# Performance work log

Measured on AMD Instinct MI355X. Metric: run time of the kernel, lower is better.

The kernel has to match this reference:

```python
import jax, jax.numpy as jnp
import numpy as np

B, T, S = 1, 8, 1024
HID, H = 1152, 16
D = HID // H  # 72
EPS = 1e-6


def rmsnorm(t, gamma):
    # t: [b,t,s,h,d], gamma: [h,d] per-head learnable scale (QKNorm)
    var = jnp.mean(jnp.square(t), axis=-1, keepdims=True)
    return t * jax.lax.rsqrt(var + EPS) * gamma


def setup_inputs() -> dict:
    key = jax.random.key(0)
    ks = jax.random.split(key, 8)
    sc = lambda fan_in: 1.0 / np.sqrt(fan_in)
    x = jax.random.normal(ks[0], (B, T, S, HID), dtype=jnp.float32)
    Wq = jax.random.normal(ks[1], (HID, HID), dtype=jnp.float32) * sc(HID)
    bq = jnp.zeros((HID,), dtype=jnp.float32)
    Wkv = jax.random.normal(ks[2], (HID, 2 * HID), dtype=jnp.float32) * sc(HID)
    bkv = jnp.zeros((2 * HID,), dtype=jnp.float32)
    q_gamma = jnp.ones((H, D), dtype=jnp.float32)
    k_gamma = jnp.ones((H, D), dtype=jnp.float32)
    Wo = jax.random.normal(ks[3], (HID, HID), dtype=jnp.float32) * sc(HID)
    return {"x": x, "Wq": Wq, "bq": bq, "Wkv": Wkv, "bkv": bkv,
            "q_gamma": q_gamma, "k_gamma": k_gamma, "Wo": Wo}


def reference(x, Wq, bq, Wkv, bkv, q_gamma, k_gamma, Wo):
    b, t, s, _ = x.shape
    q = (x @ Wq + bq).reshape(b, t, s, H, D)
    kv = x @ Wkv + bkv
    k, v = jnp.split(kv, 2, axis=-1)
    k = k.reshape(b, t, s, H, D)
    v = v.reshape(b, t, s, H, D)
    q = rmsnorm(q, q_gamma)
    k = rmsnorm(k, k_gamma)
    # NOTE: original applies no 1/sqrt(d) scaling (QKNorm replaces it)
    attn_weight = jnp.einsum('btqhd,btkhd->bthqk', q, k)
    attn = jax.nn.softmax(attn_weight, axis=-1)
    out = jnp.einsum('bthqk,btkhd->btqhd', attn, v).reshape(b, t, s, HID)
    return out @ Wo
```

## Files before the change

### kernel.cpp

```cpp
#include <hip/hip_runtime.h>


typedef __attribute__((ext_vector_type(4))) short s16x4;
typedef __attribute__((ext_vector_type(8))) short s16x8;
typedef __attribute__((ext_vector_type(4))) float f32x4;
typedef __attribute__((ext_vector_type(16))) float f32x16;
typedef __attribute__((ext_vector_type(4))) int i32x4;

__device__ __forceinline__ unsigned short f2b(float x) {
  unsigned u = __float_as_uint(x);
  u += 0x7FFFu + ((u >> 16) & 1u);
  return (unsigned short)(u >> 16);
}
__device__ __forceinline__ float b2f(unsigned short u) {
  return __uint_as_float(((unsigned)u) << 16);
}
__device__ __forceinline__ void gld16(const void* g, void* l) {
  __builtin_amdgcn_global_load_lds(
      (const __attribute__((address_space(1))) void*)g,
      (__attribute__((address_space(3))) void*)l, 16, 0, 0);
}

__global__ __launch_bounds__(256) void cvt_bf16_kernel(const float* __restrict__ in,
                                                       unsigned short* __restrict__ out,
                                                       int n16) {
  int i = blockIdx.x * 256 + threadIdx.x;
  if (i >= n16) return;
  const float4* p = (const float4*)(in + (size_t)i * 16);
  float4 a = p[0], b = p[1], c = p[2], d = p[3];
  s16x8 r0, r1;
  r0[0] = (short)f2b(a.x); r0[1] = (short)f2b(a.y); r0[2] = (short)f2b(a.z); r0[3] = (short)f2b(a.w);
  r0[4] = (short)f2b(c.x); r0[5] = (short)f2b(c.y); r0[6] = (short)f2b(c.z); r0[7] = (short)f2b(c.w);
  r1[0] = (short)f2b(b.x); r1[1] = (short)f2b(b.y); r1[2] = (short)f2b(b.z); r1[3] = (short)f2b(b.w);
  r1[4] = (short)f2b(d.x); r1[5] = (short)f2b(d.y); r1[6] = (short)f2b(d.z); r1[7] = (short)f2b(d.w);
  *(s16x8*)(out + (size_t)i * 16) = r0;
  *(s16x8*)(out + (size_t)i * 16 + 8) = r1;
}

__global__ __launch_bounds__(256) void transpose_cvt_kernel(const float* __restrict__ W,
                                                            unsigned short* __restrict__ WT,
                                                            int K, int N) {
  __shared__ float tile[32][33];
  int n0 = blockIdx.x * 32, k0 = blockIdx.y * 32;
  int tx = threadIdx.x, ty = threadIdx.y;
#pragma unroll
  for (int i = 0; i < 4; i++)
    tile[ty + i * 8][tx] = W[(size_t)(k0 + ty + i * 8) * N + n0 + tx];
  __syncthreads();
  int stx = (tx & 19) | ((tx & 4) << 1) | ((tx & 8) >> 1);
#pragma unroll
  for (int i = 0; i < 4; i++)
    WT[(size_t)(n0 + ty + i * 8) * K + k0 + stx] = f2b(tile[tx][ty + i * 8]);
}

__global__ __launch_bounds__(256) void gemm_qkv_kernel(const unsigned short* __restrict__ A,
                                                       const unsigned short* __restrict__ BT,
                                                       const float* __restrict__ biasq,
                                                       const float* __restrict__ biaskv,
                                                       unsigned short* __restrict__ qn,
                                                       unsigned short* __restrict__ kn,
                                                       unsigned short* __restrict__ vt) {
  constexpr int K = 1152;
  constexpr int NT = K / 32;
  __shared__ __align__(16) unsigned short LDSU[3 * 8192 + 3 * 4096];
  unsigned short* As = LDSU;
  unsigned short* Bs = LDSU + 3 * 8192;
  int tid = threadIdx.x;
  int lane = tid & 63, wave = tid >> 6;
  int wr = (wave >> 1) * 128, wc = (wave & 1) * 64;
  int l31 = lane & 31, lh = lane >> 5;
  int bid = blockIdx.x;
  int xcd = bid & 7;
  int w = bid >> 3;
  int st = w / 12, inner = w - st * 12;
  int ibx = inner % 3, iby = inner / 3;
  int bx = st * 3 + ibx;
  int by = xcd * 4 + iby;
  int brow = by * 256, bcol = bx * 128;
  const unsigned short* AsrcP[4];
  const unsigned short* BsrcP[2];
  int dstA[4], dstB[2];
#pragma unroll
  for (int i = 0; i < 4; i++) {
    int c = tid + 256 * i;
    int row = c >> 2, j = c & 3;
    AsrcP[i] = A + (size_t)(brow + row) * K + (j ^ ((row >> 1) & 3)) * 8;
    dstA[i] = (wave * 64 + 256 * i) * 8;
  }
#pragma unroll
  for (int i = 0; i < 2; i++) {
    int c = tid + 256 * i;
    int row = c >> 2, j = c & 3;
    BsrcP[i] = BT + (size_t)(bcol + row) * K + (j ^ ((row >> 1) & 3)) * 8;
    dstB[i] = (wave * 64 + 256 * i) * 8;
  }
#define STAGE(KT, BUF)                                           \
  {                                                              \
    int kb = (KT) * 32;                                          \
    gld16(AsrcP[0] + kb, &As[(BUF) * 8192 + dstA[0]]);           \
    gld16(AsrcP[1] + kb, &As[(BUF) * 8192 + dstA[1]]);           \
    gld16(AsrcP[2] + kb, &As[(BUF) * 8192 + dstA[2]]);           \
    gld16(AsrcP[3] + kb, &As[(BUF) * 8192 + dstA[3]]);           \
    gld16(BsrcP[0] + kb, &Bs[(BUF) * 4096 + dstB[0]]);           \
    gld16(BsrcP[1] + kb, &Bs[(BUF) * 4096 + dstB[1]]);           \
  }
  int fr = (l31 >> 1) & 3;
  int slotk[2] = {(lh ^ fr) * 8, ((2 + lh) ^ fr) * 8};
  STAGE(0, 0);
  STAGE(1, 1);
  f32x16 acc[4][2] = {};
  int cur = 0;
  for (int kt = 0; kt < NT; kt++) {
    if (kt < NT - 1)
      asm volatile("s_waitcnt vmcnt(6)\n\ts_barrier" ::: "memory");
    else
      asm volatile("s_waitcnt vmcnt(0)\n\ts_barrier" ::: "memory");
    if (kt + 2 < NT) {
      int nb = (cur == 0) ? 2 : cur - 1;
      STAGE(kt + 2, nb);
    }
    int ab = cur * 8192, bb = cur * 4096;
#pragma unroll
    for (int kk = 0; kk < 2; kk++) {
      int so = slotk[kk];
      s16x8 af[4], bf[2];
#pragma unroll
      for (int m = 0; m < 4; m++)
        af[m] = *(const s16x8*)&As[ab + (wr + m * 32 + l31) * 32 + so];
#pragma unroll
      for (int n = 0; n < 2; n++)
        bf[n] = *(const s16x8*)&Bs[bb + (wc + n * 32 + l31) * 32 + so];
      __builtin_amdgcn_s_setprio(1);
#pragma unroll
      for (int m = 0; m < 4; m++)
#pragma unroll
        for (int n = 0; n < 2; n++)
          acc[m][n] = __builtin_amdgcn_mfma_f32_32x32x16_bf16(af[m], bf[n], acc[m][n], 0, 0, 0);
      __builtin_amdgcn_s_setprio(0);
    }
    cur = (cur == 2) ? 0 : cur + 1;
  }
#undef STAGE
  if (bcol >= 2304) {
    __syncthreads();
    int c0 = bcol - 2304;
#pragma unroll
    for (int m = 0; m < 4; m++) {
#pragma unroll
      for (int n = 0; n < 2; n++) {
        int col = wc + n * 32 + l31;
        float bias = biaskv[1152 + c0 + col];
#pragma unroll
        for (int reg = 0; reg < 16; reg++) {
          int row = wr + m * 32 + (reg & 3) + 8 * (reg >> 2) + 4 * lh;
          LDSU[col * 264 + row] = f2b(acc[m][n][reg] + bias);
        }
      }
    }
    __syncthreads();
    int t = brow >> 10, sbase = brow & 1023;
#pragma unroll
    for (int i = 0; i < 16; i++) {
      int id = tid + 256 * i;
      int col = id >> 5, rowc = id & 31;
      int c = c0 + col;
      int h = c / 72, d = c - h * 72;
      s16x8 v8 = *(const s16x8*)&LDSU[col * 264 + rowc * 8];
      *(s16x8*)(vt + ((size_t)((t * 16 + h) * 80 + d)) * 1024 + sbase + rowc * 8) = v8;
    }
  } else {
#pragma unroll
    for (int m = 0; m < 4; m++) {
#pragma unroll
      for (int n = 0; n < 2; n++) {
        int gcol = bcol + wc + n * 32 + l31;
        float bias = (gcol < 1152) ? biasq[gcol] : biaskv[gcol - 1152];
        int c = (gcol < 1152) ? gcol : gcol - 1152;
        int h = c / 72, d = c - h * 72;
        unsigned short* dst = (gcol < 1152) ? qn : kn;
#pragma unroll
        for (int reg = 0; reg < 16; reg++) {
          int grow = brow + wr + m * 32 + (reg & 3) + 8 * (reg >> 2) + 4 * lh;
          float v = acc[m][n][reg] + bias;
          int t = grow >> 10, s = grow & 1023;
          dst[((size_t)((t * 16 + h) * 1024 + s)) * 96 + d] = f2b(v);
        }
      }
    }
  }
}

__global__ __launch_bounds__(256) void gemm_out_kernel(const unsigned short* __restrict__ A,
                                                       const unsigned short* __restrict__ BT,
                                                       int N, int gx,
                                                       float* __restrict__ outF) {
  constexpr int K = 1152;
  constexpr int NT = K / 32;
  __shared__ __align__(16) unsigned short As[3 * 4096];
  __shared__ __align__(16) unsigned short Bs[3 * 4096];
  int tid = threadIdx.x;
  int lane = tid & 63, wave = tid >> 6;
  int wr = (wave >> 1) * 64, wc = (wave & 1) * 64;
  int l31 = lane & 31, lh = lane >> 5;
  int bid = blockIdx.x;
  int xcd = bid & 7;
  int w = bid >> 3;
  int st = w / 24, inner = w - st * 24;
  int ibx = inner % 3, iby = inner / 3;
  int bx = st * 3 + ibx;
  int by = xcd * 8 + iby;
  int brow = by * 128, bcol = bx * 128;
  const unsigned short* AsrcP[2];
  const unsigned short* BsrcP[2];
  int dst0[2];
#pragma unroll
  for (int i = 0; i < 2; i++) {
    int c = tid + 256 * i;
    int row = c >> 2, j = c & 3;
    int ch = j ^ ((row >> 1) & 3);
    AsrcP[i] = A + (size_t)(brow + row) * K + ch * 8;
    BsrcP[i] = BT + (size_t)(bcol + row) * K + ch * 8;
    dst0[i] = (wave * 64 + 256 * i) * 8;
  }
#define STAGE(KT, BUF)                                          \
  {                                                             \
    int kb = (KT) * 32;                                         \
    gld16(AsrcP[0] + kb, &As[(BUF) * 4096 + dst0[0]]);          \
    gld16(BsrcP[0] + kb, &Bs[(BUF) * 4096 + dst0[0]]);          \
    gld16(AsrcP[1] + kb, &As[(BUF) * 4096 + dst0[1]]);          \
    gld16(BsrcP[1] + kb, &Bs[(BUF) * 4096 + dst0[1]]);          \
  }
  int fr = (l31 >> 1) & 3;
  int slotk[2] = {(lh ^ fr) * 8, ((2 + lh) ^ fr) * 8};
  STAGE(0, 0);
  STAGE(1, 1);
  f32x16 acc[2][2] = {};
  int cur = 0;
  for (int kt = 0; kt < NT; kt++) {
    if (kt < NT - 1)
      asm volatile("s_waitcnt vmcnt(4)\n\ts_barrier" ::: "memory");
    else
      asm volatile("s_waitcnt vmcnt(0)\n\ts_barrier" ::: "memory");
    if (kt + 2 < NT) {
      int nb = (cur == 0) ? 2 : cur - 1;
      STAGE(kt + 2, nb);
    }
    int ab = cur * 4096;
#pragma unroll
    for (int kk = 0; kk < 2; kk++) {
      int so = slotk[kk];
      s16x8 af[2], bf[2];
#pragma unroll
      for (int m = 0; m < 2; m++)
        af[m] = *(const s16x8*)&As[ab + (wr + m * 32 + l31) * 32 + so];
#pragma unroll
      for (int n = 0; n < 2; n++)
        bf[n] = *(const s16x8*)&Bs[ab + (wc + n * 32 + l31) * 32 + so];
      __builtin_amdgcn_s_setprio(1);
#pragma unroll
      for (int m = 0; m < 2; m++)
#pragma unroll
        for (int n = 0; n < 2; n++)
          acc[m][n] = __builtin_amdgcn_mfma_f32_32x32x16_bf16(af[m], bf[n], acc[m][n], 0, 0, 0);
      __builtin_amdgcn_s_setprio(0);
    }
    cur = (cur == 2) ? 0 : cur + 1;
  }
#undef STAGE
#pragma unroll
  for (int m = 0; m < 2; m++) {
#pragma unroll
    for (int n = 0; n < 2; n++) {
#pragma unroll
      for (int reg = 0; reg < 16; reg++) {
        int grow = brow + wr + m * 32 + (reg & 3) + 8 * (reg >> 2) + 4 * lh;
        int gcol = bcol + wc + n * 32 + l31;
        outF[(size_t)grow * N + gcol] = acc[m][n][reg];
      }
    }
  }
}

__global__ __launch_bounds__(256) void rmsnorm2_kernel(unsigned short* __restrict__ qn,
                                                       unsigned short* __restrict__ kn,
                                                       const float* __restrict__ qg,
                                                       const float* __restrict__ kg) {
  int r = blockIdx.x * 4 + (threadIdx.x >> 6);
  int isK = r >= 131072;
  int g = isK ? r - 131072 : r;
  unsigned short* buf = isK ? kn : qn;
  const float* gamma = isK ? kg : qg;
  int h = (g >> 10) & 15;
  size_t base = (size_t)g * 96;
  int l = threadIdx.x & 63;
  float e0 = b2f(buf[base + l]);
  float e1 = 0.f;
  if (l < 8) e1 = b2f(buf[base + 64 + l]);
  float ss = e0 * e0 + e1 * e1;
#pragma unroll
  for (int m = 1; m < 64; m <<= 1) ss += __shfl_xor(ss, m);
  float sc = rsqrtf(ss * (1.0f / 72.0f) + 1e-6f);
  buf[base + l] = f2b(e0 * sc * gamma[h * 72 + l]);
  if (l < 32) {
    float v = 0.f;
    if (l < 8) v = e1 * sc * gamma[h * 72 + 64 + l];
    buf[base + 64 + l] = f2b(v);
  }
}

__global__ __launch_bounds__(256) void attn_kernel(const unsigned short* __restrict__ Qn,
                                                   const unsigned short* __restrict__ Kn,
                                                   const unsigned short* __restrict__ VtG,
                                                   unsigned short* __restrict__ att) {
  __shared__ unsigned short Kl[2][64][100];
  __shared__ unsigned short Vt[2][80][76];
  int tid = threadIdx.x;
  int lane = tid & 63, wave = tid >> 6;
  int l15 = lane & 15, lq = lane >> 4, kf = lq * 4;
  int bid = blockIdx.x;
  int orig = (bid & 7) * 128 + (bid >> 3);
  int qb = orig & 7, th = orig >> 3;
  int t = th >> 4, h = th & 15;
  const unsigned short* Q = Qn + (size_t)th * 1024 * 96;
  const unsigned short* Kp = Kn + (size_t)th * 1024 * 96;
  const unsigned short* Vg = VtG + (size_t)th * 80 * 1024;
  int qrow0 = qb * 128 + wave * 32;
  int krow[3], kco[3], vd[3], vco[3];
#pragma unroll
  for (int i = 0; i < 3; i++) {
    int c = tid + i * 256;
    krow[i] = c / 12;
    kco[i] = c - 12 * krow[i];
    int cc = tid + i * 256;
    vd[i] = cc >> 3;
    vco[i] = cc & 7;
  }
  bool v2 = tid < 128;
  s16x8 sk[3], sv[3];
  s16x8 qf0[3], qf1[3];
#pragma unroll
  for (int c = 0; c < 3; c++) {
    const unsigned short* p0 = Q + (size_t)(qrow0 + l15) * 96 + c * 32 + kf;
    s16x4 lo = *(const s16x4*)p0;
    s16x4 hi = *(const s16x4*)(p0 + 16);
    qf0[c] = __builtin_shufflevector(lo, hi, 0, 1, 2, 3, 4, 5, 6, 7);
    const unsigned short* p1 = Q + (size_t)(qrow0 + 16 + l15) * 96 + c * 32 + kf;
    s16x4 lo1 = *(const s16x4*)p1;
    s16x4 hi1 = *(const s16x4*)(p1 + 16);
    qf1[c] = __builtin_shufflevector(lo1, hi1, 0, 1, 2, 3, 4, 5, 6, 7);
  }
  f32x4 o[2][5] = {};
  float m_r[2] = {-3.0e38f, -3.0e38f}, l_r[2] = {0.f, 0.f};

#pragma unroll
  for (int i = 0; i < 3; i++)
    sk[i] = *(const s16x8*)(Kp + (size_t)krow[i] * 96 + kco[i] * 8);
#pragma unroll
  for (int i = 0; i < 2; i++)
    sv[i] = *(const s16x8*)(Vg + (size_t)vd[i] * 1024 + vco[i] * 8);
  if (v2) sv[2] = *(const s16x8*)(Vg + (size_t)vd[2] * 1024 + vco[2] * 8);
#pragma unroll
  for (int i = 0; i < 3; i++) *(s16x8*)&Kl[0][krow[i]][kco[i] * 8] = sk[i];
#pragma unroll
  for (int i = 0; i < 2; i++) *(s16x8*)&Vt[0][vd[i]][vco[i] * 8] = sv[i];
  if (v2) *(s16x8*)&Vt[0][vd[2]][vco[2] * 8] = sv[2];

  for (int tt = 0; tt < 16; tt++) {
    __syncthreads();
    int cur = tt & 1;
    if (tt < 15) {
      int kv1 = (tt + 1) * 64;
#pragma unroll
      for (int i = 0; i < 3; i++)
        sk[i] = *(const s16x8*)(Kp + (size_t)(kv1 + krow[i]) * 96 + kco[i] * 8);
#pragma unroll
      for (int i = 0; i < 2; i++)
        sv[i] = *(const s16x8*)(Vg + (size_t)vd[i] * 1024 + kv1 + vco[i] * 8);
      if (v2) sv[2] = *(const s16x8*)(Vg + (size_t)vd[2] * 1024 + kv1 + vco[2] * 8);
    }
    f32x4 st0[4], st1[4];
    __builtin_amdgcn_s_setprio(1);
#pragma unroll
    for (int n = 0; n < 4; n++) {
      f32x4 a0 = {}, a1 = {};
#pragma unroll
      for (int c = 0; c < 3; c++) {
        s16x4 lo = *(const s16x4*)&Kl[cur][n * 16 + l15][c * 32 + kf];
        s16x4 hi = *(const s16x4*)&Kl[cur][n * 16 + l15][c * 32 + kf + 16];
        s16x8 kfr = __builtin_shufflevector(lo, hi, 0, 1, 2, 3, 4, 5, 6, 7);
        a0 = __builtin_amdgcn_mfma_f32_16x16x32_bf16(kfr, qf0[c], a0, 0, 0, 0);
        a1 = __builtin_amdgcn_mfma_f32_16x16x32_bf16(kfr, qf1[c], a1, 0, 0, 0);
      }
      st0[n] = a0;
      st1[n] = a1;
    }
    __builtin_amdgcn_s_setprio(0);
#define SOFTMAX(ST, G)                                                        \
    {                                                                         \
      float tmax = ST[0][0];                                                  \
      _Pragma("unroll") for (int n = 0; n < 4; n++)                           \
        _Pragma("unroll") for (int r = 0; r < 4; r++)                         \
          tmax = fmaxf(tmax, ST[n][r]);                                       \
      tmax = fmaxf(tmax, __shfl_xor(tmax, 16));                               \
      tmax = fmaxf(tmax, __shfl_xor(tmax, 32));                               \
      float mn = fmaxf(m_r[G], tmax);                                         \
      float scale = __expf(m_r[G] - mn);                                      \
      m_r[G] = mn;                                                            \
      float sum = 0.f;                                                        \
      _Pragma("unroll") for (int n = 0; n < 4; n++)                           \
        _Pragma("unroll") for (int r = 0; r < 4; r++) {                       \
          float p = __expf(ST[n][r] - mn);                                    \
          ST[n][r] = p;                                                       \
          sum += p;                                                           \
        }                                                                     \
      sum += __shfl_xor(sum, 16);                                             \
      sum += __shfl_xor(sum, 32);                                             \
      l_r[G] = l_r[G] * scale + sum;                                          \
      _Pragma("unroll") for (int r = 0; r < 4; r++) {                         \
        float scq = __shfl(scale, 4 * lq + r);                                \
        _Pragma("unroll") for (int v = 0; v < 5; v++) o[G][v][r] *= scq;      \
      }                                                                       \
    }
#define PV(ST, G)                                                             \
    {                                                                         \
      __builtin_amdgcn_s_setprio(1);                                          \
      _Pragma("unroll") for (int b = 0; b < 2; b++) {                         \
        int w0, w1, w2, w3;                                                   \
        asm("v_cvt_pk_bf16_f32 %0, %1, %2" : "=v"(w0)                         \
            : "v"(ST[2 * b][0]), "v"(ST[2 * b][1]));                          \
        asm("v_cvt_pk_bf16_f32 %0, %1, %2" : "=v"(w1)                         \
            : "v"(ST[2 * b][2]), "v"(ST[2 * b][3]));                          \
        asm("v_cvt_pk_bf16_f32 %0, %1, %2" : "=v"(w2)                         \
            : "v"(ST[2 * b + 1][0]), "v"(ST[2 * b + 1][1]));                  \
        asm("v_cvt_pk_bf16_f32 %0, %1, %2" : "=v"(w3)                         \
            : "v"(ST[2 * b + 1][2]), "v"(ST[2 * b + 1][3]));                  \
        i32x4 pw = {w0, w1, w2, w3};                                          \
        s16x8 pf = __builtin_bit_cast(s16x8, pw);                             \
        _Pragma("unroll") for (int v = 0; v < 5; v++) {                       \
          s16x4 vlo = *(const s16x4*)&Vt[cur][v * 16 + l15][b * 32 + kf];     \
          s16x4 vhi = *(const s16x4*)&Vt[cur][v * 16 + l15][b * 32 + kf + 16];\
          s16x8 vf = __builtin_shufflevector(vlo, vhi, 0, 1, 2, 3, 4, 5, 6, 7);\
          o[G][v] = __builtin_amdgcn_mfma_f32_16x16x32_bf16(pf, vf, o[G][v], 0, 0, 0); \
        }                                                                     \
      }                                                                       \
      __builtin_amdgcn_s_setprio(0);                                          \
    }
    SOFTMAX(st0, 0);
    PV(st0, 0);
    SOFTMAX(st1, 1);
    PV(st1, 1);
#undef SOFTMAX
#undef PV
    if (tt < 15) {
      int nxt = cur ^ 1;
#pragma unroll
      for (int i = 0; i < 3; i++) *(s16x8*)&Kl[nxt][krow[i]][kco[i] * 8] = sk[i];
#pragma unroll
      for (int i = 0; i < 2; i++) *(s16x8*)&Vt[nxt][vd[i]][vco[i] * 8] = sv[i];
      if (v2) *(s16x8*)&Vt[nxt][vd[2]][vco[2] * 8] = sv[2];
    }
  }
#pragma unroll
  for (int g = 0; g < 2; g++)
#pragma unroll
    for (int r = 0; r < 4; r++) {
      float inv = 1.0f / __shfl(l_r[g], 4 * lq + r);
      int qrow = qrow0 + g * 16 + 4 * lq + r;
      size_t rowbase = (size_t)(t * 1024 + qrow) * 1152;
#pragma unroll
      for (int v = 0; v < 5; v++) {
        int d = v * 16 + l15;
        if (d < 72) {
          int col = h * 72 + d;
          int scol = (col & ~12) | ((col & 4) << 1) | ((col & 8) >> 1);
          att[rowbase + scol] = f2b(o[g][v][r] * inv);
        }
      }
    }
}

extern "C" void kernel_launch(void* const* d_in, const int* in_sizes, int n_in,
                              void* d_out, int out_size, void* d_ws, size_t ws_size,
                              hipStream_t stream) {
  const float* x   = (const float*)d_in[0];
  const float* Wq  = (const float*)d_in[1];
  const float* bq  = (const float*)d_in[2];
  const float* Wkv = (const float*)d_in[3];
  const float* bkv = (const float*)d_in[4];
  const float* qg  = (const float*)d_in[5];
  const float* kg  = (const float*)d_in[6];
  const float* Wo  = (const float*)d_in[7];
  float* out = (float*)d_out;

  char* w = (char*)d_ws;
  unsigned short* xb   = (unsigned short*)w; w += (size_t)8192 * 1152 * 2;
  unsigned short* WqT  = (unsigned short*)w; w += (size_t)1152 * 1152 * 2;
  unsigned short* WkvT = (unsigned short*)w; w += (size_t)2304 * 1152 * 2;
  unsigned short* WoT  = (unsigned short*)w; w += (size_t)1152 * 1152 * 2;
  unsigned short* qn   = (unsigned short*)w; w += (size_t)128 * 1024 * 96 * 2;
  unsigned short* kn   = (unsigned short*)w; w += (size_t)128 * 1024 * 96 * 2;
  unsigned short* vt   = (unsigned short*)w; w += (size_t)128 * 80 * 1024 * 2;
  unsigned short* att  = (unsigned short*)w; w += (size_t)8192 * 1152 * 2;

  cvt_bf16_kernel<<<2304, 256, 0, stream>>>(x, xb, 9437184 / 16);
  transpose_cvt_kernel<<<dim3(36, 36), dim3(32, 8), 0, stream>>>(Wq, WqT, 1152, 1152);
  transpose_cvt_kernel<<<dim3(72, 36), dim3(32, 8), 0, stream>>>(Wkv, WkvT, 1152, 2304);
  transpose_cvt_kernel<<<dim3(36, 36), dim3(32, 8), 0, stream>>>(Wo, WoT, 1152, 1152);

  gemm_qkv_kernel<<<864, 256, 0, stream>>>(xb, WqT, bq, bkv, qn, kn, vt);
  rmsnorm2_kernel<<<65536, 256, 0, stream>>>(qn, kn, qg, kg);

  attn_kernel<<<1024, 256, 0, stream>>>(qn, kn, vt, att);

  gemm_out_kernel<<<576, 256, 0, stream>>>(att, WoT, 1152, 9, out);
}
```

Measured before the change: 302.1 us.

## Merge weight transposes into one launch, single-buffer V, skip softmax rescale

The three weight transpose-convert launches become one kernel that picks its matrix from the block index, which saves launch overhead. In the attention kernel the V shared tile drops from double to single buffering, with an extra barrier before the next V tile is written, to cut LDS use and possibly raise occupancy. The online softmax now skips the rescale of the running max and accumulators when no row max grows, decided by a wave-wide vote. The extra barrier adds a synchronisation point each iteration, and the vote adds branching.

```diff
diff --git a/kernel.cpp b/kernel.cpp
--- a/kernel.cpp
+++ b/kernel.cpp
@@ -37,12 +37,23 @@
   *(s16x8*)(out + (size_t)i * 16 + 8) = r1;
 }
 
-__global__ __launch_bounds__(256) void transpose_cvt_kernel(const float* __restrict__ W,
-                                                            unsigned short* __restrict__ WT,
-                                                            int K, int N) {
+__global__ __launch_bounds__(256) void transpose_cvt3_kernel(
+    const float* __restrict__ Wq, const float* __restrict__ Wkv,
+    const float* __restrict__ Wo, unsigned short* __restrict__ WqT,
+    unsigned short* __restrict__ WkvT, unsigned short* __restrict__ WoT) {
+  constexpr int K = 1152;
+  int id = blockIdx.x;
+  const float* W;
+  unsigned short* WT;
+  int N;
+  if (id < 1296) { W = Wq; WT = WqT; N = 1152; }
+  else if (id < 3888) { W = Wkv; WT = WkvT; N = 2304; id -= 1296; }
+  else { W = Wo; WT = WoT; N = 1152; id -= 3888; }
+  int ntiles = N / 32;
+  int bxx = id % ntiles, byy = id / ntiles;
   __shared__ float tile[32][33];
-  int n0 = blockIdx.x * 32, k0 = blockIdx.y * 32;
-  int tx = threadIdx.x, ty = threadIdx.y;
+  int n0 = bxx * 32, k0 = byy * 32;
+  int tx = threadIdx.x & 31, ty = threadIdx.x >> 5;
 #pragma unroll
   for (int i = 0; i < 4; i++)
     tile[ty + i * 8][tx] = W[(size_t)(k0 + ty + i * 8) * N + n0 + tx];
@@ -313,7 +324,7 @@
                                                    const unsigned short* __restrict__ VtG,
                                                    unsigned short* __restrict__ att) {
   __shared__ unsigned short Kl[2][64][100];
-  __shared__ unsigned short Vt[2][80][76];
+  __shared__ unsigned short Vt[80][76];
   int tid = threadIdx.x;
   int lane = tid & 63, wave = tid >> 6;
   int l15 = lane & 15, lq = lane >> 4, kf = lq * 4;
@@ -362,8 +373,8 @@
 #pragma unroll
   for (int i = 0; i < 3; i++) *(s16x8*)&Kl[0][krow[i]][kco[i] * 8] = sk[i];
 #pragma unroll
-  for (int i = 0; i < 2; i++) *(s16x8*)&Vt[0][vd[i]][vco[i] * 8] = sv[i];
-  if (v2) *(s16x8*)&Vt[0][vd[2]][vco[2] * 8] = sv[2];
+  for (int i = 0; i < 2; i++) *(s16x8*)&Vt[vd[i]][vco[i] * 8] = sv[i];
+  if (v2) *(s16x8*)&Vt[vd[2]][vco[2] * 8] = sv[2];
 
   for (int tt = 0; tt < 16; tt++) {
     __syncthreads();
@@ -403,22 +414,30 @@
           tmax = fmaxf(tmax, ST[n][r]);                                       \
       tmax = fmaxf(tmax, __shfl_xor(tmax, 16));                               \
       tmax = fmaxf(tmax, __shfl_xor(tmax, 32));                               \
-      float mn = fmaxf(m_r[G], tmax);                                         \
-      float scale = __expf(m_r[G] - mn);                                      \
-      m_r[G] = mn;                                                            \
+      bool up = !__all(tmax <= m_r[G]);                                       \
+      float scale = 1.0f;                                                     \
+      if (up) {                                                               \
+        float mn = fmaxf(m_r[G], tmax);                                       \
+        scale = __expf(m_r[G] - mn);                                          \
+        m_r[G] = mn;                                                          \
+      }                                                                       \
       float sum = 0.f;                                                        \
       _Pragma("unroll") for (int n = 0; n < 4; n++)                           \
         _Pragma("unroll") for (int r = 0; r < 4; r++) {                       \
-          float p = __expf(ST[n][r] - mn);                                    \
+          float p = __expf(ST[n][r] - m_r[G]);                                \
           ST[n][r] = p;                                                       \
           sum += p;                                                           \
         }                                                                     \
       sum += __shfl_xor(sum, 16);                                             \
       sum += __shfl_xor(sum, 32);                                             \
-      l_r[G] = l_r[G] * scale + sum;                                          \
-      _Pragma("unroll") for (int r = 0; r < 4; r++) {                         \
-        float scq = __shfl(scale, 4 * lq + r);                                \
-        _Pragma("unroll") for (int v = 0; v < 5; v++) o[G][v][r] *= scq;      \
+      if (up) {                                                               \
+        l_r[G] = l_r[G] * scale + sum;                                        \
+        _Pragma("unroll") for (int r = 0; r < 4; r++) {                       \
+          float scq = __shfl(scale, 4 * lq + r);                              \
+          _Pragma("unroll") for (int v = 0; v < 5; v++) o[G][v][r] *= scq;    \
+        }                                                                     \
+      } else {                                                                \
+        l_r[G] += sum;                                                        \
       }                                                                       \
     }
 #define PV(ST, G)                                                             \
@@ -437,8 +456,8 @@
         i32x4 pw = {w0, w1, w2, w3};                                          \
         s16x8 pf = __builtin_bit_cast(s16x8, pw);                             \
         _Pragma("unroll") for (int v = 0; v < 5; v++) {                       \
-          s16x4 vlo = *(const s16x4*)&Vt[cur][v * 16 + l15][b * 32 + kf];     \
-          s16x4 vhi = *(const s16x4*)&Vt[cur][v * 16 + l15][b * 32 + kf + 16];\
+          s16x4 vlo = *(const s16x4*)&Vt[v * 16 + l15][b * 32 + kf];          \
+          s16x4 vhi = *(const s16x4*)&Vt[v * 16 + l15][b * 32 + kf + 16];     \
           s16x8 vf = __builtin_shufflevector(vlo, vhi, 0, 1, 2, 3, 4, 5, 6, 7);\
           o[G][v] = __builtin_amdgcn_mfma_f32_16x16x32_bf16(pf, vf, o[G][v], 0, 0, 0); \
         }                                                                     \
@@ -452,12 +471,13 @@
 #undef SOFTMAX
 #undef PV
     if (tt < 15) {
+      __syncthreads();
       int nxt = cur ^ 1;
 #pragma unroll
       for (int i = 0; i < 3; i++) *(s16x8*)&Kl[nxt][krow[i]][kco[i] * 8] = sk[i];
 #pragma unroll
-      for (int i = 0; i < 2; i++) *(s16x8*)&Vt[nxt][vd[i]][vco[i] * 8] = sv[i];
-      if (v2) *(s16x8*)&Vt[nxt][vd[2]][vco[2] * 8] = sv[2];
+      for (int i = 0; i < 2; i++) *(s16x8*)&Vt[vd[i]][vco[i] * 8] = sv[i];
+      if (v2) *(s16x8*)&Vt[vd[2]][vco[2] * 8] = sv[2];
     }
   }
 #pragma unroll
@@ -503,9 +523,7 @@
   unsigned short* att  = (unsigned short*)w; w += (size_t)8192 * 1152 * 2;
 
   cvt_bf16_kernel<<<2304, 256, 0, stream>>>(x, xb, 9437184 / 16);
-  transpose_cvt_kernel<<<dim3(36, 36), dim3(32, 8), 0, stream>>>(Wq, WqT, 1152, 1152);
-  transpose_cvt_kernel<<<dim3(72, 36), dim3(32, 8), 0, stream>>>(Wkv, WkvT, 1152, 2304);
-  transpose_cvt_kernel<<<dim3(36, 36), dim3(32, 8), 0, stream>>>(Wo, WoT, 1152, 1152);
+  transpose_cvt3_kernel<<<5184, 256, 0, stream>>>(Wq, Wkv, Wo, WqT, WkvT, WoT);
 
   gemm_qkv_kernel<<<864, 256, 0, stream>>>(xb, WqT, bq, bkv, qn, kn, vt);
   rmsnorm2_kernel<<<65536, 256, 0, stream>>>(qn, kn, qg, kg);
```

Result: no change. 302.4 us (+0.1%).
